# Optimization experiments

Measured on AMD Instinct MI355X. Metric: run time of the kernel, lower is better.

Reference implementation:

```python
import jax, jax.numpy as jnp
import numpy as np

H = 16          # num_attention_heads
D = 64          # head dim (hidden 1024 / 16)
ATT_SPAN = 512  # max_relative_positions (no bucketing)
EPS = 1e-5      # layer_norm_eps


def setup_inputs() -> dict:
    key = jax.random.key(0)
    ks = jax.random.split(key, 12)
    B, S, Hd = 1, 2048, 1024
    std = 0.02
    inp = {
        "hidden_states": jax.random.normal(ks[0], (B, S, Hd), jnp.float32),
        "attention_mask": jnp.ones((B, 1, S, S), jnp.bool_),
        "rel_embeddings": jax.random.normal(ks[1], (2 * ATT_SPAN, Hd), jnp.float32) * std,
        "Wq": jax.random.normal(ks[2], (Hd, Hd), jnp.float32) * std,
        "bq": jnp.zeros((Hd,), jnp.float32),
        "Wk": jax.random.normal(ks[3], (Hd, Hd), jnp.float32) * std,
        "bk": jnp.zeros((Hd,), jnp.float32),
        "Wv": jax.random.normal(ks[4], (Hd, Hd), jnp.float32) * std,
        "bv": jnp.zeros((Hd,), jnp.float32),
        "Wo": jax.random.normal(ks[5], (Hd, Hd), jnp.float32) * std,
        "bo": jnp.zeros((Hd,), jnp.float32),
        "ln_g": jnp.ones((Hd,), jnp.float32),
        "ln_b": jnp.zeros((Hd,), jnp.float32),
    }
    return inp


def _attention(hidden_states, attention_mask, rel_embeddings,
               Wq, bq, Wk, bk, Wv, bv, Wo, bo, ln_g, ln_b):
    B, S, Hd = hidden_states.shape
    dtype = hidden_states.dtype

    def split_heads(x):  # [B,S,Hd] -> [B,H,S,D]
        return x.reshape(B, S, H, D).transpose(0, 2, 1, 3)

    q = split_heads(hidden_states @ Wq + bq)
    k = split_heads(hidden_states @ Wk + bk)
    v = split_heads(hidden_states @ Wv + bv)

    # scale_factor = 1 + len(pos_att_type) = 3 (c2p + p2c)
    scale = jnp.sqrt(jnp.asarray(D * 3, dtype))
    scores = jnp.einsum('bhqd,bhkd->bhqk', q, k) / scale

    # relative positions: rel_pos[i,j] = i - j (query - key)
    ids = jnp.arange(S)
    rel_pos = ids[:, None] - ids[None, :]  # [S,S] int

    # shared attention key: project rel embeddings with the same q/k projections
    pos_k = (rel_embeddings @ Wk + bk).reshape(2 * ATT_SPAN, H, D).transpose(1, 0, 2)  # [H,2K,D]
    pos_q = (rel_embeddings @ Wq + bq).reshape(2 * ATT_SPAN, H, D).transpose(1, 0, 2)  # [H,2K,D]

    # content-to-position
    c2p = jnp.einsum('bhqd,hkd->bhqk', q, pos_k)                    # [B,H,S,2K]
    c2p_idx = jnp.clip(rel_pos + ATT_SPAN, 0, 2 * ATT_SPAN - 1)     # [S,S]
    c2p = jnp.take_along_axis(c2p, c2p_idx[None, None], axis=-1)    # [B,H,S,S]

    # position-to-content (computed over key positions, then transposed)
    p2c = jnp.einsum('bhkd,hqd->bhkq', k, pos_q)                    # [B,H,S,2K]
    p2c_idx = jnp.clip(-rel_pos + ATT_SPAN, 0, 2 * ATT_SPAN - 1)    # [S,S]
    p2c = jnp.take_along_axis(p2c, p2c_idx[None, None], axis=-1)    # [B,H,S,S]
    p2c = jnp.swapaxes(p2c, -1, -2)

    scores = scores + (c2p + p2c) / scale

    # XSoftmax: mask with -inf, softmax, re-zero masked positions
    neg = jnp.finfo(dtype).min
    scores = jnp.where(attention_mask, scores, neg)
    probs = jax.nn.softmax(scores, axis=-1)
    probs = jnp.where(attention_mask, probs, jnp.asarray(0.0, dtype))

    ctx = jnp.einsum('bhqk,bhkd->bhqd', probs, v)
    ctx = ctx.transpose(0, 2, 1, 3).reshape(B, S, Hd)

    # SEWDSelfOutput: dense + residual + LayerNorm
    out = ctx @ Wo + bo
    x = out + hidden_states
    mu = x.mean(-1, keepdims=True)
    var = ((x - mu) ** 2).mean(-1, keepdims=True)
    return (x - mu) / jnp.sqrt(var + EPS) * ln_g + ln_b


def reference(hidden_states, attention_mask, rel_embeddings,
              Wq, bq, Wk, bk, Wv, bv, Wo, bo, ln_g, ln_b):
    return _attention(hidden_states, attention_mask, rel_embeddings,
                      Wq, bq, Wk, bk, Wv, bv, Wo, bo, ln_g, ln_b)
```

## Files before the change

### kernel.cpp

```cpp
#include <hip/hip_runtime.h>
#include <hip/hip_bf16.h>
#include <cstdint>
#include <cstddef>

typedef __attribute__((ext_vector_type(8))) short bf16x8;
typedef __attribute__((ext_vector_type(4))) short bf16x4;
typedef __attribute__((ext_vector_type(4))) float f32x4;
typedef __attribute__((ext_vector_type(4))) unsigned short u16x4;
typedef unsigned short u16;
typedef unsigned int u32;

__device__ __forceinline__ float bf2f(u16 v) {
    union { u32 u; float f; } c; c.u = ((u32)v) << 16; return c.f;
}
__device__ __forceinline__ u16 f2bf(float f) {
    union { float f; u32 u; } c; c.f = f;
    u32 u = c.u;
    return (u16)((u + 0x7FFFu + ((u >> 16) & 1u)) >> 16);
}

#define MFMA16(a, b, c) __builtin_amdgcn_mfma_f32_16x16x32_bf16((a), (b), (c), 0, 0, 0)

#if __has_builtin(__builtin_amdgcn_mfma_f32_16x16x16bf16_1k)
#define MFMA1K(a, b, c) __builtin_amdgcn_mfma_f32_16x16x16bf16_1k((a), (b), (c), 0, 0, 0)
#define MFMA1K_ASM 0
#else
__device__ __forceinline__ f32x4 mfma1k_asm(bf16x4 a, bf16x4 b, f32x4 c) {
    asm volatile("v_mfma_f32_16x16x16_bf16 %0, %1, %2, %0" : "+v"(c) : "v"(a), "v"(b));
    return c;
}
#define MFMA1K(a, b, c) mfma1k_asm((a), (b), (c))
#define MFMA1K_ASM 1
#endif

#if __has_builtin(__builtin_amdgcn_exp2f)
#define EXP2F(x) __builtin_amdgcn_exp2f(x)
#else
#define EXP2F(x) exp2f(x)
#endif

union U8 { u16 h[8]; uint4 v; };

__device__ __forceinline__ U8 cvt8(float4 a, float4 b) {
    U8 u;
    u.h[0] = f2bf(a.x); u.h[1] = f2bf(a.y); u.h[2] = f2bf(a.z); u.h[3] = f2bf(a.w);
    u.h[4] = f2bf(b.x); u.h[5] = f2bf(b.y); u.h[6] = f2bf(b.z); u.h[7] = f2bf(b.w);
    return u;
}

struct TArgs { const float* src[4]; u16* dst[4]; };

__global__ __launch_bounds__(256)
void transpose_kernel(TArgs ta)
{
    __shared__ float T[64][65];
    const float* W = ta.src[blockIdx.z];
    u16* Wt = ta.dst[blockIdx.z];
    const int tid = threadIdx.x;
    const int bx = blockIdx.x, by = blockIdx.y;
    const int rr = tid >> 4, c4 = (tid & 15) * 4;
#pragma unroll
    for (int i = 0; i < 4; ++i) {
        int r = rr + i * 16;
        float4 v = *(const float4*)(W + (size_t)(by * 64 + r) * 1024 + bx * 64 + c4);
        T[r][c4] = v.x; T[r][c4 + 1] = v.y; T[r][c4 + 2] = v.z; T[r][c4 + 3] = v.w;
    }
    __syncthreads();
#pragma unroll
    for (int i = 0; i < 4; ++i) {
        int n = rr + i * 16;
        u16 o0 = f2bf(T[c4][n]), o1 = f2bf(T[c4 + 1][n]);
        u16 o2 = f2bf(T[c4 + 2][n]), o3 = f2bf(T[c4 + 3][n]);
        uint2 pk;
        pk.x = (u32)o0 | ((u32)o1 << 16);
        pk.y = (u32)o2 | ((u32)o3 << 16);
        *(uint2*)(Wt + (size_t)(bx * 64 + n) * 1024 + by * 64 + c4) = pk;
    }
}

struct GArgs {
    const u16* Bt[3];
    const float* bias[3];
    void* out[3];
    int mode[3];
};

__global__ __launch_bounds__(256, 4)
void gemm_nt_kernel(const void* __restrict__ Av, int abf, GArgs ga,
                    const float* __restrict__ resid, int M, int K,
                    int bcol0, int Nout)
{
    const int z = blockIdx.z;
    const u16* Bt = ga.Bt[z];
    const float* bias = ga.bias[z];
    void* Cout = ga.out[z];
    const int mode = ga.mode[z];

    __shared__ __align__(16) u16 As[64 * 72];
    __shared__ __align__(16) u16 Bs[64 * 72];
    const int tid = threadIdx.x;
    const int bm = blockIdx.y * 64, bn = blockIdx.x * 64;
    const int wave = tid >> 6, lane = tid & 63;
    const int quad = lane >> 4, l16 = lane & 15;
    const int wm = (wave >> 1) * 32, wn = (wave & 1) * 32;
    const int ar = tid >> 2, ac = (tid & 3) * 16;

    f32x4 acc[2][2] = {};

    for (int k0 = 0; k0 < K; k0 += 64) {
        uint4 a0v, a1v;
        if (abf) {
            const u16* A16 = (const u16*)Av + (size_t)(bm + ar) * K + k0 + ac;
            a0v = *(const uint4*)A16;
            a1v = *(const uint4*)(A16 + 8);
        } else {
            const float* ap = (const float*)Av + (size_t)(bm + ar) * K + k0 + ac;
            a0v = cvt8(*(const float4*)ap, *(const float4*)(ap + 4)).v;
            a1v = cvt8(*(const float4*)(ap + 8), *(const float4*)(ap + 12)).v;
        }
        const u16* btp = Bt + (size_t)(bcol0 + bn + ar) * K + k0 + ac;
        uint4 b0v = *(const uint4*)btp;
        uint4 b1v = *(const uint4*)(btp + 8);
        __syncthreads();
        *(uint4*)(As + ar * 72 + ac) = a0v;
        *(uint4*)(As + ar * 72 + ac + 8) = a1v;
        *(uint4*)(Bs + ar * 72 + ac) = b0v;
        *(uint4*)(Bs + ar * 72 + ac + 8) = b1v;
        __syncthreads();
#pragma unroll
        for (int kh = 0; kh < 64; kh += 32) {
            bf16x8 a0 = *(const bf16x8*)(As + (wm + l16) * 72 + kh + quad * 8);
            bf16x8 a1 = *(const bf16x8*)(As + (wm + 16 + l16) * 72 + kh + quad * 8);
            bf16x8 b0 = *(const bf16x8*)(Bs + (wn + l16) * 72 + kh + quad * 8);
            bf16x8 b1 = *(const bf16x8*)(Bs + (wn + 16 + l16) * 72 + kh + quad * 8);
            acc[0][0] = MFMA16(a0, b0, acc[0][0]);
            acc[0][1] = MFMA16(a0, b1, acc[0][1]);
            acc[1][0] = MFMA16(a1, b0, acc[1][0]);
            acc[1][1] = MFMA16(a1, b1, acc[1][1]);
        }
    }

#pragma unroll
    for (int i = 0; i < 2; ++i) {
#pragma unroll
        for (int j = 0; j < 2; ++j) {
            int col = bn + wn + j * 16 + l16;
            float bb = bias[bcol0 + col];
#pragma unroll
            for (int r = 0; r < 4; ++r) {
                int row = bm + wm + i * 16 + quad * 4 + r;
                float v = acc[i][j][r] + bb;
                if (mode == 0) {
                    ((u16*)Cout)[(size_t)row * Nout + col] = f2bf(v);
                } else if (mode == 1) {
                    ((u16*)Cout)[(size_t)col * M + row] = f2bf(v);
                } else {
                    ((float*)Cout)[(size_t)row * Nout + col] = v + resid[(size_t)row * Nout + col];
                }
            }
        }
    }
}

__global__ __launch_bounds__(256)
void consts_kernel(const u16* __restrict__ Qg, const u16* __restrict__ Kg,
                   const u16* __restrict__ posKg, const u16* __restrict__ posQg,
                   float* __restrict__ cst, int ld)
{
    const int s = blockIdx.x * 256 + threadIdx.x;
    const int hg = blockIdx.y;
    float d0 = 0.f, d1 = 0.f, d2 = 0.f, d3 = 0.f;
#pragma unroll
    for (int c = 0; c < 64; c += 8) {
        U8 q, k, p0, p1, r0, r1;
        q.v  = *(const uint4*)(Qg + (size_t)s * ld + hg * 64 + c);
        k.v  = *(const uint4*)(Kg + (size_t)s * ld + hg * 64 + c);
        p0.v = *(const uint4*)(posKg + (size_t)0 * ld + hg * 64 + c);
        p1.v = *(const uint4*)(posKg + (size_t)1023 * ld + hg * 64 + c);
        r0.v = *(const uint4*)(posQg + (size_t)0 * ld + hg * 64 + c);
        r1.v = *(const uint4*)(posQg + (size_t)1023 * ld + hg * 64 + c);
#pragma unroll
        for (int j = 0; j < 8; ++j) {
            float qq = bf2f(q.h[j]), kk = bf2f(k.h[j]);
            d0 += qq * bf2f(p0.h[j]);
            d1 += qq * bf2f(p1.h[j]);
            d2 += kk * bf2f(r0.h[j]);
            d3 += kk * bf2f(r1.h[j]);
        }
    }
    cst[(size_t)(hg * 4 + 0) * 2048 + s] = d0;
    cst[(size_t)(hg * 4 + 1) * 2048 + s] = d1;
    cst[(size_t)(hg * 4 + 2) * 2048 + s] = d2;
    cst[(size_t)(hg * 4 + 3) * 2048 + s] = d3;
}

__global__ __launch_bounds__(256, 2)
void attn_kernel(const u16* __restrict__ Qg, const u16* __restrict__ Kg,
                 const u16* __restrict__ Vtg, const u16* __restrict__ posKg,
                 const u16* __restrict__ posQg, const float* __restrict__ cst,
                 u16* __restrict__ ctx, int h0, int ld)
{
    __shared__ __align__(16) u16 Ks[64 * 72];
    __shared__ __align__(16) u16 Vs[64 * 72];
    __shared__ __align__(16) u16 pKs[128 * 72];
    __shared__ __align__(16) u16 pQs[128 * 72];
    __shared__ __align__(16) u16 bandC[4 * 16 * 72];
    __shared__ __align__(16) u16 bandP[16 * 264];
    const int tid = threadIdx.x;

    int hg, qi;
    if (gridDim.y == 16) {
        const int b = blockIdx.x + (blockIdx.y << 5);
        const int xcd = b & 7, r = b >> 3;
        hg = (xcd << 1) | (r & 1);
        qi = r >> 1;
    } else {
        hg = blockIdx.y; qi = blockIdx.x;
    }
    const int q0 = qi * 64;
    const int wave = tid >> 6, lane = tid & 63, quad = lane >> 4, l16 = lane & 15;
    const float CSC = 0.07216878364870322f * 1.44269504f;

    bf16x8 aq0 = *(const bf16x8*)(Qg + (q0 + wave * 16 + l16) * ld + hg * 64 + quad * 8);
    bf16x8 aq1 = *(const bf16x8*)(Qg + (q0 + wave * 16 + l16) * ld + hg * 64 + 32 + quad * 8);

    float cq0s = 0.f, cq1s = 0.f;
    if (cst) {
        int qgl = q0 + wave * 16 + l16;
        cq0s = cst[(hg * 4 + 0) * 2048 + qgl];
        cq1s = cst[(hg * 4 + 1) * 2048 + qgl];
    }

    const int sm0 = tid >> 3, sd0 = (tid & 7) * 8;
    const int sm1 = sm0 + 32;

    auto isfar = [&](int kt) {
        const int d = kt - q0;
        return cst && (d >= 576 || d <= -576);
    };

    auto stage = [&](int kt, bool withpos) {
        const u16* kgb = Kg + hg * 64 + sd0;
        const u16* vgb = Vtg + kt + sd0;
        uint4 k0 = *(const uint4*)(kgb + (kt + sm0) * ld);
        uint4 k1 = *(const uint4*)(kgb + (kt + sm1) * ld);
        uint4 v0 = *(const uint4*)(vgb + (hg * 64 + sm0) * 2048);
        uint4 v1 = *(const uint4*)(vgb + (hg * 64 + sm1) * 2048);
        if (withpos) {
            const int kap = q0 - kt + 449;
            int r0 = kap + sm0;      r0 = r0 < 0 ? 0 : (r0 > 1023 ? 1023 : r0);
            int r1 = kap + sm0 + 32; r1 = r1 < 0 ? 0 : (r1 > 1023 ? 1023 : r1);
            int r2 = kap + sm0 + 64; r2 = r2 < 0 ? 0 : (r2 > 1023 ? 1023 : r2);
            int r3 = kap + sm0 + 96; r3 = r3 < 0 ? 0 : (r3 > 1023 ? 1023 : r3);
            const u16* pKb = posKg + hg * 64 + sd0;
            const u16* pQb = posQg + hg * 64 + sd0;
            uint4 a0 = *(const uint4*)(pKb + r0 * ld);
            uint4 a1 = *(const uint4*)(pKb + r1 * ld);
            uint4 a2 = *(const uint4*)(pKb + r2 * ld);
            uint4 a3 = *(const uint4*)(pKb + r3 * ld);
            uint4 b0 = *(const uint4*)(pQb + r0 * ld);
            uint4 b1 = *(const uint4*)(pQb + r1 * ld);
            uint4 b2 = *(const uint4*)(pQb + r2 * ld);
            uint4 b3 = *(const uint4*)(pQb + r3 * ld);
            *(uint4*)(Ks + sm0 * 72 + sd0) = k0;
            *(uint4*)(Ks + sm1 * 72 + sd0) = k1;
            *(uint4*)(Vs + sm0 * 72 + sd0) = v0;
            *(uint4*)(Vs + sm1 * 72 + sd0) = v1;
            *(uint4*)(pKs + sm0 * 72 + sd0) = a0;
            *(uint4*)(pKs + (sm0 + 32) * 72 + sd0) = a1;
            *(uint4*)(pKs + (sm0 + 64) * 72 + sd0) = a2;
            *(uint4*)(pKs + (sm0 + 96) * 72 + sd0) = a3;
            *(uint4*)(pQs + sm0 * 72 + sd0) = b0;
            *(uint4*)(pQs + (sm0 + 32) * 72 + sd0) = b1;
            *(uint4*)(pQs + (sm0 + 64) * 72 + sd0) = b2;
            *(uint4*)(pQs + (sm0 + 96) * 72 + sd0) = b3;
        } else {
            *(uint4*)(Ks + sm0 * 72 + sd0) = k0;
            *(uint4*)(Ks + sm1 * 72 + sd0) = k1;
            *(uint4*)(Vs + sm0 * 72 + sd0) = v0;
            *(uint4*)(Vs + sm1 * 72 + sd0) = v1;
        }
    };

    auto bandcomp = [&]() {
        bf16x8 aP0 = *(const bf16x8*)(Ks + (wave * 16 + l16) * 72 + quad * 8);
        bf16x8 aP1 = *(const bf16x8*)(Ks + (wave * 16 + l16) * 72 + 32 + quad * 8);
        const int iC0 = wave * 16 + l16;
        const int iP0 = 48 - wave * 16 + l16;
        u16* bC = bandC + wave * 1152;
        u16* bP = bandP;
#pragma unroll
        for (int n = 0; n < 5; ++n) {
            const u16* pK = pKs + (iC0 + n * 16) * 72;
            const u16* pQ = pQs + (iP0 + n * 16) * 72;
            bf16x8 bK0 = *(const bf16x8*)(pK + quad * 8);
            bf16x8 bK1 = *(const bf16x8*)(pK + 32 + quad * 8);
            bf16x8 bQ0 = *(const bf16x8*)(pQ + quad * 8);
            bf16x8 bQ1 = *(const bf16x8*)(pQ + 32 + quad * 8);
            f32x4 aC = {0.f, 0.f, 0.f, 0.f}, aP = {0.f, 0.f, 0.f, 0.f};
            aC = MFMA16(aq0, bK0, aC);
            aC = MFMA16(aq1, bK1, aC);
            aP = MFMA16(aP0, bQ0, aP);
            aP = MFMA16(aP1, bQ1, aP);
#pragma unroll
            for (int r = 0; r < 4; ++r) {
                int q15 = quad * 4 + r;
                int k = q15 + 63 - n * 16 - l16;
                if ((unsigned)k < 64u) bC[q15 * 72 + k] = f2bf(aC[r]);
                int qs = n * 16 + l16 + quad * 4 + r - 15;
                if ((unsigned)qs < 64u) bP[(wave * 4 + quad) * 264 + qs * 4 + r] = f2bf(aP[r]);
            }
        }
    };

    stage(0, !isfar(0));
    __syncthreads();

    f32x4 OTa[4] = {}, OTb[4] = {};
    float lr4[4] = {0.f, 0.f, 0.f, 0.f};

    for (int kt = 0; kt < 2048; kt += 64) {
        const int diff = kt - q0;
        const bool far = cst && (diff >= 576 || diff <= -576);
        const bool havenext = (kt + 64 < 2048);
        const bool nextnear = havenext && !isfar(kt + 64);

        f32x4 sT[4];
#pragma unroll
        for (int j = 0; j < 4; ++j) {
            f32x4 z = {0.f, 0.f, 0.f, 0.f};
            bf16x8 a0 = *(const bf16x8*)(Ks + (j * 16 + l16) * 72 + quad * 8);
            bf16x8 a1 = *(const bf16x8*)(Ks + (j * 16 + l16) * 72 + 32 + quad * 8);
            z = MFMA16(a0, aq0, z);
            z = MFMA16(a1, aq1, z);
            sT[j] = z;
        }

        if (!far) {
            bandcomp();
            __syncthreads();
        }

        bf16x4 pb[4];
        if (far) {
            const float cqs = (diff > 0) ? cq0s : cq1s;
            const float* pc = cst + (hg * 4 + (diff > 0 ? 2 : 3)) * 2048 + kt;
#pragma unroll
            for (int j = 0; j < 4; ++j) {
                float4 ck4 = *(const float4*)(pc + j * 16 + quad * 4);
                const float* ck = (const float*)&ck4;
#pragma unroll
                for (int r = 0; r < 4; ++r) {
                    float t = sT[j][r] + cqs + ck[r];
                    float e = EXP2F(fminf(t * CSC, 86.5f));
                    lr4[j] += e;
                    pb[j][r] = (short)f2bf(e);
                }
            }
        } else {
            const u16* bC = bandC + wave * 1152 + l16 * 72;
            const u16* bP = bandP + (wave * 16 + l16) * 4;
#pragma unroll
            for (int j = 0; j < 4; ++j) {
                u16x4 c4 = *(const u16x4*)(bC + j * 16 + quad * 4);
                u16x4 p4 = *(const u16x4*)(bP + (j * 4 + quad) * 264);
#pragma unroll
                for (int r = 0; r < 4; ++r) {
                    float t = sT[j][r] + bf2f(c4[r]) + bf2f(p4[r]);
                    float e = EXP2F(fminf(t * CSC, 86.5f));
                    lr4[j] += e;
                    pb[j][r] = (short)f2bf(e);
                }
            }
        }

#pragma unroll
        for (int jd = 0; jd < 4; ++jd) {
            const u16* vrow = Vs + (jd * 16 + l16) * 72;
            OTa[jd] = MFMA1K(*(const bf16x4*)(vrow + quad * 4), pb[0], OTa[jd]);
            OTb[jd] = MFMA1K(*(const bf16x4*)(vrow + 16 + quad * 4), pb[1], OTb[jd]);
            OTa[jd] = MFMA1K(*(const bf16x4*)(vrow + 32 + quad * 4), pb[2], OTa[jd]);
            OTb[jd] = MFMA1K(*(const bf16x4*)(vrow + 48 + quad * 4), pb[3], OTb[jd]);
        }

        __syncthreads();
        if (havenext) {
            stage(kt + 64, nextnear);
            __syncthreads();
        }
    }

#if MFMA1K_ASM
    asm volatile("s_nop 7\n\ts_nop 7" ::);
#endif

    float lr = (lr4[0] + lr4[1]) + (lr4[2] + lr4[3]);
    lr += __shfl_xor(lr, 16, 64);
    lr += __shfl_xor(lr, 32, 64);
    float inv = 1.0f / fmaxf(lr, 1e-20f);
    const int row = q0 + wave * 16 + l16;
#pragma unroll
    for (int jd = 0; jd < 4; ++jd) {
        u16x4 o;
#pragma unroll
        for (int r = 0; r < 4; ++r) o[r] = f2bf((OTa[jd][r] + OTb[jd][r]) * inv);
        *(u16x4*)(ctx + row * 1024 + (h0 + hg) * 64 + jd * 16 + quad * 4) = o;
    }
}

__global__ __launch_bounds__(256, 4)
void ln_kernel(const float* __restrict__ x, const float* __restrict__ g,
               const float* __restrict__ b, float* __restrict__ out)
{
    const int row = blockIdx.x;
    const int tid = threadIdx.x;
    const int wave = tid >> 6, lane = tid & 63;
    const float* xr = x + (size_t)row * 1024;
    float v[4]; float s = 0.f;
#pragma unroll
    for (int i = 0; i < 4; ++i) { v[i] = xr[tid + i * 256]; s += v[i]; }
    __shared__ float red[4];
    __shared__ float red2[4];
#pragma unroll
    for (int m = 1; m < 64; m <<= 1) s += __shfl_xor(s, m, 64);
    if (lane == 0) red[wave] = s;
    __syncthreads();
    float mu = (red[0] + red[1] + red[2] + red[3]) * (1.f / 1024.f);
    float vs = 0.f;
#pragma unroll
    for (int i = 0; i < 4; ++i) { float d = v[i] - mu; vs += d * d; }
#pragma unroll
    for (int m = 1; m < 64; m <<= 1) vs += __shfl_xor(vs, m, 64);
    if (lane == 0) red2[wave] = vs;
    __syncthreads();
    float var = (red2[0] + red2[1] + red2[2] + red2[3]) * (1.f / 1024.f);
    float rstd = rsqrtf(var + 1e-5f);
#pragma unroll
    for (int i = 0; i < 4; ++i) {
        int c = tid + i * 256;
        out[(size_t)row * 1024 + c] = (v[i] - mu) * rstd * g[c] + b[c];
    }
}

extern "C" void kernel_launch(void* const* d_in, const int* in_sizes, int n_in,
                              void* d_out, int out_size, void* d_ws, size_t ws_size,
                              hipStream_t stream)
{
    const float* hs  = (const float*)d_in[0];
    const float* rel = (const float*)d_in[2];
    const float* Wq  = (const float*)d_in[3];
    const float* bq  = (const float*)d_in[4];
    const float* Wk  = (const float*)d_in[5];
    const float* bk  = (const float*)d_in[6];
    const float* Wv  = (const float*)d_in[7];
    const float* bv  = (const float*)d_in[8];
    const float* Wo  = (const float*)d_in[9];
    const float* bo  = (const float*)d_in[10];
    const float* lng = (const float*)d_in[11];
    const float* lnb = (const float*)d_in[12];

    u16* Wqt = (u16*)d_out;
    u16* Wkt = Wqt + (size_t)1024 * 1024;
    u16* Wvt = Wkt + (size_t)1024 * 1024;
    u16* Wot = Wvt + (size_t)1024 * 1024;
    float* cst = (float*)d_out;

    const size_t MB = 1024 * 1024;
    size_t fixed = 256 + 4 * MB + 4096;
    int G = 1;
    if (ws_size > fixed + MB) {
        size_t g = (ws_size - fixed) / MB;
        G = g > 16 ? 16 : (int)g;
    }
    if (G < 1) G = 1;

    char* w = (char*)d_ws;
    size_t off = 0;
    auto take = [&](size_t n) { void* p = w + off; off = (off + n + 255) & ~(size_t)255; return p; };
    (void)take(256);
    u16* ctx = (u16*)take((size_t)2048 * 1024 * 2);
    float* xalt = nullptr;
    if (G < 8) {
        size_t budget = (ws_size > fixed + 8 * MB) ? (ws_size - fixed - 8 * MB) / MB : 1;
        G = budget < 1 ? 1 : (budget > 16 ? 16 : (int)budget);
        xalt = (float*)take((size_t)2048 * 1024 * 4);
    }
    u16* Qg    = (u16*)take((size_t)2048 * 64 * G * 2);
    u16* Kg    = (u16*)take((size_t)2048 * 64 * G * 2);
    u16* Vtg   = (u16*)take((size_t)64 * G * 2048 * 2);
    u16* posKg = (u16*)take((size_t)1024 * 64 * G * 2);
    u16* posQg = (u16*)take((size_t)1024 * 64 * G * 2);
    float* x = xalt ? xalt : (float*)Qg;

    dim3 blk(256);

    TArgs ta;
    ta.src[0] = Wq; ta.src[1] = Wk; ta.src[2] = Wv; ta.src[3] = Wo;
    ta.dst[0] = Wqt; ta.dst[1] = Wkt; ta.dst[2] = Wvt; ta.dst[3] = Wot;
    transpose_kernel<<<dim3(16, 16, 4), blk, 0, stream>>>(ta);

    const bool full = (G == 16);
    for (int h0 = 0; h0 < 16; h0 += G) {
        int gcnt = (16 - h0) < G ? (16 - h0) : G;
        int Ng = 64 * gcnt, bc0 = 64 * h0;

        GArgs qa;
        qa.Bt[0] = Wqt; qa.bias[0] = bq; qa.out[0] = Qg;  qa.mode[0] = 0;
        qa.Bt[1] = Wkt; qa.bias[1] = bk; qa.out[1] = Kg;  qa.mode[1] = 0;
        qa.Bt[2] = Wvt; qa.bias[2] = bv; qa.out[2] = Vtg; qa.mode[2] = 1;
        gemm_nt_kernel<<<dim3(gcnt, 32, 3), blk, 0, stream>>>(hs, 0, qa, nullptr, 2048, 1024, bc0, Ng);

        GArgs pa;
        pa.Bt[0] = Wkt; pa.bias[0] = bk; pa.out[0] = posKg; pa.mode[0] = 0;
        pa.Bt[1] = Wqt; pa.bias[1] = bq; pa.out[1] = posQg; pa.mode[1] = 0;
        pa.Bt[2] = Wqt; pa.bias[2] = bq; pa.out[2] = posQg; pa.mode[2] = 0;
        gemm_nt_kernel<<<dim3(gcnt, 16, 2), blk, 0, stream>>>(rel, 0, pa, nullptr, 1024, 1024, bc0, Ng);

        if (full)
            consts_kernel<<<dim3(8, G), blk, 0, stream>>>(Qg, Kg, posKg, posQg, cst, Ng);

        attn_kernel<<<dim3(32, gcnt), blk, 0, stream>>>(Qg, Kg, Vtg, posKg, posQg,
                                                        full ? cst : nullptr, ctx, h0, Ng);
    }

    GArgs fa;
    fa.Bt[0] = Wot; fa.bias[0] = bo; fa.out[0] = x; fa.mode[0] = 2;
    fa.Bt[1] = Wot; fa.bias[1] = bo; fa.out[1] = x; fa.mode[1] = 2;
    fa.Bt[2] = Wot; fa.bias[2] = bo; fa.out[2] = x; fa.mode[2] = 2;
    gemm_nt_kernel<<<dim3(16, 32, 1), blk, 0, stream>>>(ctx, 1, fa, hs, 2048, 1024, 0, 1024);

    ln_kernel<<<dim3(2048), blk, 0, stream>>>(x, lng, lnb, (float*)d_out);
}
```

Before: 271.0 us.

## Add 128x64 bf16 GEMM with direct global-to-LDS loads and pre-converted inputs

Adds a new GEMM kernel with a 128x64 tile that loads bf16 A and B tiles straight into XOR-swizzled LDS using global_load_lds. Hidden states and relative embeddings are first converted to bf16 in separate kernels, so the GEMM never converts from fp32 inside its loop. The QKV, positional and output projections use the new kernel when all heads fit in the workspace. The cost is two extra conversion launches and extra workspace, and the new GEMM does not double-buffer LDS.

Result: no change. 272.3 us (+0.5%).

```diff
diff --git a/kernel.cpp b/kernel.cpp
--- a/kernel.cpp
+++ b/kernel.cpp
@@ -37,6 +37,20 @@
 #define EXP2F(x) __builtin_amdgcn_exp2f(x)
 #else
 #define EXP2F(x) exp2f(x)
+#endif
+
+#if __has_builtin(__builtin_amdgcn_global_load_lds)
+#define HAVE_GLL 1
+__device__ __forceinline__ void gload16(const u16* g, u16* l, int lane) {
+    (void)lane;
+    __builtin_amdgcn_global_load_lds((__attribute__((address_space(1))) void*)(void*)g,
+                                     (__attribute__((address_space(3))) void*)l, 16, 0, 0);
+}
+#else
+#define HAVE_GLL 0
+__device__ __forceinline__ void gload16(const u16* g, u16* l, int lane) {
+    *(uint4*)(l + lane * 8) = *(const uint4*)g;
+}
 #endif
 
 union U8 { u16 h[8]; uint4 v; };
@@ -78,12 +92,97 @@
     }
 }
 
+__global__ __launch_bounds__(256)
+void cvt_bf16_kernel(const float* __restrict__ src, u16* __restrict__ dst)
+{
+    const size_t i = ((size_t)blockIdx.x * 256 + threadIdx.x) * 8;
+    float4 a = *(const float4*)(src + i);
+    float4 b = *(const float4*)(src + i + 4);
+    *(uint4*)(dst + i) = cvt8(a, b).v;
+}
+
 struct GArgs {
     const u16* Bt[3];
     const float* bias[3];
     void* out[3];
     int mode[3];
 };
+
+__global__ __launch_bounds__(256, 2)
+void gemm128_kernel(const u16* __restrict__ A, GArgs ga, const float* __restrict__ resid,
+                    int M, int bcol0, int Nout)
+{
+    const int z = blockIdx.z;
+    const u16* Bt = ga.Bt[z];
+    const float* bias = ga.bias[z];
+    void* Cout = ga.out[z];
+    const int mode = ga.mode[z];
+
+    __shared__ __align__(1024) u16 As[128 * 64];
+    __shared__ __align__(1024) u16 Bs[64 * 64];
+    const int tid = threadIdx.x;
+    const int bm = blockIdx.y * 128, bn = blockIdx.x * 64;
+    const int wave = tid >> 6, lane = tid & 63;
+    const int quad = lane >> 4, l16 = lane & 15;
+    const int wr = wave * 32;
+    const int srow = lane >> 3;
+    const int scol = ((lane & 7) ^ srow) * 8;
+
+    const u16* Ab = A + (size_t)(bm + srow) * 1024 + scol;
+    const u16* Bb = Bt + (size_t)(bcol0 + bn + srow) * 1024 + scol;
+
+    f32x4 acc[2][4] = {};
+
+    for (int k0 = 0; k0 < 1024; k0 += 64) {
+        __syncthreads();
+#pragma unroll
+        for (int i = 0; i < 4; ++i)
+            gload16(Ab + (size_t)(wave * 32 + i * 8) * 1024 + k0,
+                    As + (wave * 32 + i * 8) * 64, lane);
+#pragma unroll
+        for (int i = 0; i < 2; ++i)
+            gload16(Bb + (size_t)(wave * 16 + i * 8) * 1024 + k0,
+                    Bs + (wave * 16 + i * 8) * 64, lane);
+        __syncthreads();
+#pragma unroll
+        for (int kh = 0; kh < 2; ++kh) {
+            const int chunk = ((kh * 4 + quad) ^ (l16 & 7)) * 8;
+            bf16x8 af[2], bf[4];
+#pragma unroll
+            for (int mi = 0; mi < 2; ++mi)
+                af[mi] = *(const bf16x8*)(As + (wr + mi * 16 + l16) * 64 + chunk);
+#pragma unroll
+            for (int ni = 0; ni < 4; ++ni)
+                bf[ni] = *(const bf16x8*)(Bs + (ni * 16 + l16) * 64 + chunk);
+#pragma unroll
+            for (int mi = 0; mi < 2; ++mi)
+#pragma unroll
+                for (int ni = 0; ni < 4; ++ni)
+                    acc[mi][ni] = MFMA16(af[mi], bf[ni], acc[mi][ni]);
+        }
+    }
+
+#pragma unroll
+    for (int mi = 0; mi < 2; ++mi)
+#pragma unroll
+        for (int ni = 0; ni < 4; ++ni) {
+            int col = bn + ni * 16 + l16;
+            float bb = bias[bcol0 + col];
+#pragma unroll
+            for (int r = 0; r < 4; ++r) {
+                int row = bm + wr + mi * 16 + quad * 4 + r;
+                float v = acc[mi][ni][r] + bb;
+                if (mode == 0) {
+                    ((u16*)Cout)[(size_t)row * Nout + col] = f2bf(v);
+                } else if (mode == 1) {
+                    ((u16*)Cout)[(size_t)col * M + row] = f2bf(v);
+                } else {
+                    size_t idx = (size_t)row * Nout + col;
+                    ((float*)Cout)[idx] = v + resid[idx];
+                }
+            }
+        }
+}
 
 __global__ __launch_bounds__(256, 4)
 void gemm_nt_kernel(const void* __restrict__ Av, int abf, GArgs ga,
@@ -492,6 +591,18 @@
     u16* posQg = (u16*)take((size_t)1024 * 64 * G * 2);
     float* x = xalt ? xalt : (float*)Qg;
 
+    const bool full = (G == 16);
+
+    u16* hsb = nullptr; u16* relb = nullptr;
+    if (full && HAVE_GLL) {
+        size_t need = (size_t)2048 * 1024 * 2 + (size_t)1024 * 1024 * 2 + 1024;
+        if (off + need <= ws_size) {
+            hsb  = (u16*)take((size_t)2048 * 1024 * 2);
+            relb = (u16*)take((size_t)1024 * 1024 * 2);
+        }
+    }
+    const bool fastg = (hsb != nullptr);
+
     dim3 blk(256);
 
     TArgs ta;
@@ -499,35 +610,61 @@
     ta.dst[0] = Wqt; ta.dst[1] = Wkt; ta.dst[2] = Wvt; ta.dst[3] = Wot;
     transpose_kernel<<<dim3(16, 16, 4), blk, 0, stream>>>(ta);
 
-    const bool full = (G == 16);
-    for (int h0 = 0; h0 < 16; h0 += G) {
-        int gcnt = (16 - h0) < G ? (16 - h0) : G;
-        int Ng = 64 * gcnt, bc0 = 64 * h0;
+    if (fastg) {
+        cvt_bf16_kernel<<<dim3(1024), blk, 0, stream>>>(hs, hsb);
+        cvt_bf16_kernel<<<dim3(512), blk, 0, stream>>>(rel, relb);
 
         GArgs qa;
         qa.Bt[0] = Wqt; qa.bias[0] = bq; qa.out[0] = Qg;  qa.mode[0] = 0;
         qa.Bt[1] = Wkt; qa.bias[1] = bk; qa.out[1] = Kg;  qa.mode[1] = 0;
         qa.Bt[2] = Wvt; qa.bias[2] = bv; qa.out[2] = Vtg; qa.mode[2] = 1;
-        gemm_nt_kernel<<<dim3(gcnt, 32, 3), blk, 0, stream>>>(hs, 0, qa, nullptr, 2048, 1024, bc0, Ng);
+        gemm128_kernel<<<dim3(16, 16, 3), blk, 0, stream>>>(hsb, qa, nullptr, 2048, 0, 1024);
 
         GArgs pa;
         pa.Bt[0] = Wkt; pa.bias[0] = bk; pa.out[0] = posKg; pa.mode[0] = 0;
         pa.Bt[1] = Wqt; pa.bias[1] = bq; pa.out[1] = posQg; pa.mode[1] = 0;
         pa.Bt[2] = Wqt; pa.bias[2] = bq; pa.out[2] = posQg; pa.mode[2] = 0;
-        gemm_nt_kernel<<<dim3(gcnt, 16, 2), blk, 0, stream>>>(rel, 0, pa, nullptr, 1024, 1024, bc0, Ng);
-
-        if (full)
-            consts_kernel<<<dim3(8, G), blk, 0, stream>>>(Qg, Kg, posKg, posQg, cst, Ng);
-
-        attn_kernel<<<dim3(32, gcnt), blk, 0, stream>>>(Qg, Kg, Vtg, posKg, posQg,
-                                                        full ? cst : nullptr, ctx, h0, Ng);
-    }
-
-    GArgs fa;
-    fa.Bt[0] = Wot; fa.bias[0] = bo; fa.out[0] = x; fa.mode[0] = 2;
-    fa.Bt[1] = Wot; fa.bias[1] = bo; fa.out[1] = x; fa.mode[1] = 2;
-    fa.Bt[2] = Wot; fa.bias[2] = bo; fa.out[2] = x; fa.mode[2] = 2;
-    gemm_nt_kernel<<<dim3(16, 32, 1), blk, 0, stream>>>(ctx, 1, fa, hs, 2048, 1024, 0, 1024);
+        gemm128_kernel<<<dim3(16, 8, 2), blk, 0, stream>>>(relb, pa, nullptr, 1024, 0, 1024);
+
+        consts_kernel<<<dim3(8, 16), blk, 0, stream>>>(Qg, Kg, posKg, posQg, cst, 1024);
+
+        attn_kernel<<<dim3(32, 16), blk, 0, stream>>>(Qg, Kg, Vtg, posKg, posQg,
+                                                      cst, ctx, 0, 1024);
+
+        GArgs fa;
+        fa.Bt[0] = Wot; fa.bias[0] = bo; fa.out[0] = x; fa.mode[0] = 2;
+        fa.Bt[1] = Wot; fa.bias[1] = bo; fa.out[1] = x; fa.mode[1] = 2;
+        fa.Bt[2] = Wot; fa.bias[2] = bo; fa.out[2] = x; fa.mode[2] = 2;
+        gemm128_kernel<<<dim3(16, 16, 1), blk, 0, stream>>>(ctx, fa, hs, 2048, 0, 1024);
+    } else {
+        for (int h0 = 0; h0 < 16; h0 += G) {
+            int gcnt = (16 - h0) < G ? (16 - h0) : G;
+            int Ng = 64 * gcnt, bc0 = 64 * h0;
+
+            GArgs qa;
+            qa.Bt[0] = Wqt; qa.bias[0] = bq; qa.out[0] = Qg;  qa.mode[0] = 0;
+            qa.Bt[1] = Wkt; qa.bias[1] = bk; qa.out[1] = Kg;  qa.mode[1] = 0;
+            qa.Bt[2] = Wvt; qa.bias[2] = bv; qa.out[2] = Vtg; qa.mode[2] = 1;
+            gemm_nt_kernel<<<dim3(gcnt, 32, 3), blk, 0, stream>>>(hs, 0, qa, nullptr, 2048, 1024, bc0, Ng);
+
+            GArgs pa;
+            pa.Bt[0] = Wkt; pa.bias[0] = bk; pa.out[0] = posKg; pa.mode[0] = 0;
+            pa.Bt[1] = Wqt; pa.bias[1] = bq; pa.out[1] = posQg; pa.mode[1] = 0;
+            pa.Bt[2] = Wqt; pa.bias[2] = bq; pa.out[2] = posQg; pa.mode[2] = 0;
+            gemm_nt_kernel<<<dim3(gcnt, 16, 2), blk, 0, stream>>>(rel, 0, pa, nullptr, 1024, 1024, bc0, Ng);
+
+            if (full)
+                consts_kernel<<<dim3(8, G), blk, 0, stream>>>(Qg, Kg, posKg, posQg, cst, Ng);
+
+            attn_kernel<<<dim3(32, gcnt), blk, 0, stream>>>(Qg, Kg, Vtg, posKg, posQg,
+                                                            full ? cst : nullptr, ctx, h0, Ng);
+        }
+        GArgs fa;
+        fa.Bt[0] = Wot; fa.bias[0] = bo; fa.out[0] = x; fa.mode[0] = 2;
+        fa.Bt[1] = Wot; fa.bias[1] = bo; fa.out[1] = x; fa.mode[1] = 2;
+        fa.Bt[2] = Wot; fa.bias[2] = bo; fa.out[2] = x; fa.mode[2] = 2;
+        gemm_nt_kernel<<<dim3(16, 32, 1), blk, 0, stream>>>(ctx, 1, fa, hs, 2048, 1024, 0, 1024);
+    }
 
     ln_kernel<<<dim3(2048), blk, 0, stream>>>(x, lng, lnb, (float*)d_out);
 }
```

## Prefetch next K/V and positional tiles into registers before compute

Applied to the files above, without the earlier changes.

Global loads for the next key-tile's K, V and (when near-band) pos_K/pos_Q rows now go into registers at the top of each iteration, and the LDS stores happen after the end-of-iteration barrier. A sched_barrier stops the compiler from moving those loads below the MFMA work. This hides global memory latency behind the score, softmax and PV compute instead of stalling in the stage call. It costs up to 12 extra uint4 registers per thread, which may lower occupancy.

Result: no change. 266.5 us (-1.6%).

```diff
diff --git a/kernel.cpp b/kernel.cpp
--- a/kernel.cpp
+++ b/kernel.cpp
@@ -325,6 +325,37 @@
         const bool havenext = (kt + 64 < 2048);
         const bool nextnear = havenext && !isfar(kt + 64);
 
+        uint4 nk0, nk1, nv0, nv1, na0, na1, na2, na3, nb0, nb1, nb2, nb3;
+        if (havenext) {
+            const int ktn = kt + 64;
+            const u16* kgb = Kg + hg * 64 + sd0;
+            const u16* vgb = Vtg + ktn + sd0;
+            nk0 = *(const uint4*)(kgb + (ktn + sm0) * ld);
+            nk1 = *(const uint4*)(kgb + (ktn + sm1) * ld);
+            nv0 = *(const uint4*)(vgb + (hg * 64 + sm0) * 2048);
+            nv1 = *(const uint4*)(vgb + (hg * 64 + sm1) * 2048);
+            if (nextnear) {
+                const int kap = q0 - ktn + 449;
+                int r0 = kap + sm0;      r0 = r0 < 0 ? 0 : (r0 > 1023 ? 1023 : r0);
+                int r1 = kap + sm0 + 32; r1 = r1 < 0 ? 0 : (r1 > 1023 ? 1023 : r1);
+                int r2 = kap + sm0 + 64; r2 = r2 < 0 ? 0 : (r2 > 1023 ? 1023 : r2);
+                int r3 = kap + sm0 + 96; r3 = r3 < 0 ? 0 : (r3 > 1023 ? 1023 : r3);
+                const u16* pKb = posKg + hg * 64 + sd0;
+                const u16* pQb = posQg + hg * 64 + sd0;
+                na0 = *(const uint4*)(pKb + r0 * ld);
+                na1 = *(const uint4*)(pKb + r1 * ld);
+                na2 = *(const uint4*)(pKb + r2 * ld);
+                na3 = *(const uint4*)(pKb + r3 * ld);
+                nb0 = *(const uint4*)(pQb + r0 * ld);
+                nb1 = *(const uint4*)(pQb + r1 * ld);
+                nb2 = *(const uint4*)(pQb + r2 * ld);
+                nb3 = *(const uint4*)(pQb + r3 * ld);
+            }
+        }
+#if __has_builtin(__builtin_amdgcn_sched_barrier)
+        __builtin_amdgcn_sched_barrier(0);
+#endif
+
         f32x4 sT[4];
 #pragma unroll
         for (int j = 0; j < 4; ++j) {
@@ -385,7 +416,20 @@
 
         __syncthreads();
         if (havenext) {
-            stage(kt + 64, nextnear);
+            *(uint4*)(Ks + sm0 * 72 + sd0) = nk0;
+            *(uint4*)(Ks + sm1 * 72 + sd0) = nk1;
+            *(uint4*)(Vs + sm0 * 72 + sd0) = nv0;
+            *(uint4*)(Vs + sm1 * 72 + sd0) = nv1;
+            if (nextnear) {
+                *(uint4*)(pKs + sm0 * 72 + sd0) = na0;
+                *(uint4*)(pKs + (sm0 + 32) * 72 + sd0) = na1;
+                *(uint4*)(pKs + (sm0 + 64) * 72 + sd0) = na2;
+                *(uint4*)(pKs + (sm0 + 96) * 72 + sd0) = na3;
+                *(uint4*)(pQs + sm0 * 72 + sd0) = nb0;
+                *(uint4*)(pQs + (sm0 + 32) * 72 + sd0) = nb1;
+                *(uint4*)(pQs + (sm0 + 64) * 72 + sd0) = nb2;
+                *(uint4*)(pQs + (sm0 + 96) * 72 + sd0) = nb3;
+            }
             __syncthreads();
         }
     }
```
